# Optimization experiments

Hardware: AMD Instinct MI355X
Metric: run time of the kernel (lower is better)

The kernel has to match this reference:

```python
import jax, jax.numpy as jnp
import numpy as np

H = 512      # hidden_size
NH = 8       # num_attention_heads
HD = H // NH # attention_head_size
B, S = 2, 4096


def setup_inputs() -> dict:
    key = jax.random.key(0)
    ks = jax.random.split(key, 9)
    sc = 1.0 / np.sqrt(H)
    return {
        "hidden_states": jax.random.normal(ks[0], (B, S, H), dtype=jnp.float32),
        "Wq": jax.random.normal(ks[1], (H, H), dtype=jnp.float32) * sc,
        "bq": jnp.zeros((H,), dtype=jnp.float32),
        "Wk": jax.random.normal(ks[2], (H, H), dtype=jnp.float32) * sc,
        "bk": jnp.zeros((H,), dtype=jnp.float32),
        "Wv": jax.random.normal(ks[3], (H, H), dtype=jnp.float32) * sc,
        "bv": jnp.zeros((H,), dtype=jnp.float32),
        "Wo": jax.random.normal(ks[4], (H, H), dtype=jnp.float32) * sc,
        "bo": jnp.zeros((H,), dtype=jnp.float32),
    }


def reference(hidden_states, Wq, bq, Wk, bk, Wv, bv, Wo, bo):
    # QKV projections (nn.Linear: x @ W.T + b)
    def split_heads(x):  # [B,S,H] -> [B,NH,S,HD]
        return x.reshape(B, S, NH, HD).transpose(0, 2, 1, 3)

    q = split_heads(hidden_states @ Wq.T + bq)
    k = split_heads(hidden_states @ Wk.T + bk)
    v = split_heads(hidden_states @ Wv.T + bv)

    scores = jnp.einsum("bhqd,bhkd->bhqk", q, k) / np.sqrt(HD)
    probs = jax.nn.softmax(scores, axis=-1)  # dropout is identity in eval
    ctx = jnp.einsum("bhqk,bhkd->bhqd", probs, v)
    ctx = ctx.transpose(0, 2, 1, 3).reshape(B, S, H)
    return ctx @ Wo.T + bo
```

## Files before the change

kernel.cpp:

```cpp
#include <hip/hip_runtime.h>
#include <hip/hip_bf16.h>
#include <math.h>


typedef __bf16 bf16;
typedef __bf16 bf16x2v __attribute__((ext_vector_type(2)));
typedef __bf16 bf16x4 __attribute__((ext_vector_type(4)));
typedef __bf16 bf16x8 __attribute__((ext_vector_type(8)));
typedef float  f32x4  __attribute__((ext_vector_type(4)));
typedef unsigned int u32x2 __attribute__((ext_vector_type(2)));
typedef unsigned int u32x4 __attribute__((ext_vector_type(4)));

#define MFMA16(a, b, c) __builtin_amdgcn_mfma_f32_16x16x32_bf16((a), (b), (c), 0, 0, 0)

__device__ __forceinline__ void gll16(const bf16* g, bf16* l) {
    __builtin_amdgcn_global_load_lds(
        (const __attribute__((address_space(1))) void*)g,
        (__attribute__((address_space(3))) void*)l, 16, 0, 0);
}

__device__ __forceinline__ unsigned int cvtpk(float lo, float hi) {
    unsigned int r;
    asm("v_cvt_pk_bf16_f32 %0, %1, %2" : "=v"(r) : "v"(lo), "v"(hi));
    return r;
}

__global__ __launch_bounds__(256) void cvt_f32_bf16(const float* __restrict__ src,
                                                    bf16* __restrict__ dst, int n) {
    int i = (blockIdx.x * 256 + threadIdx.x) * 4;
    if (i >= n) return;
    float4 v = *reinterpret_cast<const float4*>(src + i);
    bf16x4 o = {(bf16)v.x, (bf16)v.y, (bf16)v.z, (bf16)v.w};
    *reinterpret_cast<bf16x4*>(dst + i) = o;
}

__global__ __launch_bounds__(256) void cvt_w4(const float* __restrict__ a,
                                              const float* __restrict__ b,
                                              const float* __restrict__ c,
                                              const float* __restrict__ d,
                                              bf16* __restrict__ out) {
    const int y = blockIdx.y;
    const float* src = (y == 0) ? a : (y == 1) ? b : (y == 2) ? c : d;
    int i = (blockIdx.x * 256 + threadIdx.x) * 4;
    float4 v = *reinterpret_cast<const float4*>(src + i);
    bf16x4 o = {(bf16)v.x, (bf16)v.y, (bf16)v.z, (bf16)v.w};
    *reinterpret_cast<bf16x4*>(out + y * 262144 + i) = o;
}

template <int MODE>
__global__ __launch_bounds__(256) void gemm_bt(const bf16* __restrict__ A,
                                               const bf16* __restrict__ W,
                                               const float* __restrict__ b0,
                                               const float* __restrict__ b1,
                                               const float* __restrict__ b2,
                                               bf16* __restrict__ dstbf,
                                               float* __restrict__ dstf) {
    __shared__ bf16 sA[128 * 64];
    __shared__ bf16 sB[128 * 64];

    const int tid = threadIdx.x;
    const int w   = tid >> 6;
    const int l   = tid & 63;

    int bx, by, bz;
    if (MODE == 0) {
        int lin = (blockIdx.x & 7) * 96 + (blockIdx.x >> 3);
        const int rem = lin % 12;
        bx = rem & 3; bz = rem >> 2; by = lin / 12;
    } else {
        int lin = (blockIdx.x & 7) * 32 + (blockIdx.x >> 3);
        bx = lin & 3; by = lin >> 2; bz = 0;
    }
    const int m0 = by * 128;
    const int n0 = bx * 128;
    const int z  = bz;

    const bf16*  Wz   = (MODE == 0) ? (W + z * 262144) : W;
    const float* bias = (MODE == 0) ? (z == 0 ? b0 : (z == 1 ? b1 : b2)) : b0;
    const float  scale = (MODE == 0 && z == 0) ? 0.125f * 1.4426950408889634f : 1.0f;

    const int wr = (w >> 1) * 64, wc = (w & 1) * 64;
    const int fr = l & 15, fg = l >> 4;

    const int srow0 = tid >> 3;
    const int sgr   = (tid & 7) ^ (srow0 & 7);
    const int ldso  = srow0 * 64 + (tid & 7) * 8;

    f32x4 acc[4][4];
    const f32x4 zero = {0.f, 0.f, 0.f, 0.f};
#pragma unroll
    for (int i = 0; i < 4; i++)
#pragma unroll
        for (int j = 0; j < 4; j++) acc[i][j] = zero;

    for (int kt = 0; kt < 512; kt += 64) {
        __syncthreads();
#pragma unroll
        for (int p = 0; p < 4; p++) {
            const int row = srow0 + 32 * p;
            gll16(A  + (m0 + row) * 512 + kt + sgr * 8, &sA[p * 2048 + ldso]);
            gll16(Wz + (n0 + row) * 512 + kt + sgr * 8, &sB[p * 2048 + ldso]);
        }
        __syncthreads();

#pragma unroll
        for (int ks = 0; ks < 2; ks++) {
            bf16x8 af[4], bfg[4];
#pragma unroll
            for (int mi = 0; mi < 4; mi++)
                af[mi] = *reinterpret_cast<const bf16x8*>(
                    &sA[(wr + mi * 16 + fr) * 64 + (((4 * ks + fg) ^ (fr & 7)) << 3)]);
#pragma unroll
            for (int ni = 0; ni < 4; ni++)
                bfg[ni] = *reinterpret_cast<const bf16x8*>(
                    &sB[(wc + ni * 16 + fr) * 64 + (((4 * ks + fg) ^ (fr & 7)) << 3)]);
#pragma unroll
            for (int mi = 0; mi < 4; mi++)
#pragma unroll
                for (int ni = 0; ni < 4; ni++)
                    acc[mi][ni] = MFMA16(af[mi], bfg[ni], acc[mi][ni]);
        }
    }

#pragma unroll
    for (int mi = 0; mi < 4; mi++) {
#pragma unroll
        for (int ni = 0; ni < 4; ni++) {
            const int gcol = n0 + wc + ni * 16 + fr;
            const float bc = bias[gcol];
#pragma unroll
            for (int r = 0; r < 4; r++) {
                const int grow = m0 + wr + mi * 16 + fg * 4 + r;
                float v = acc[mi][ni][r] + bc;
                if (MODE == 0) {
                    v *= scale;
                    const int bb = grow >> 12, s = grow & 4095;
                    const int hh = gcol >> 6, dd = gcol & 63;
                    size_t idx;
                    if (z == 2) {
                        idx = (size_t)2 * 4194304 +
                              ((size_t)((bb * 8 + hh) * 64 + dd)) * 4096 + s;
                    } else {
                        idx = (size_t)z * 4194304 +
                              ((size_t)((bb * 8 + hh) * 4096 + s) << 6) + dd;
                    }
                    dstbf[idx] = (bf16)v;
                } else {
                    dstf[grow * 512 + gcol] = v;
                }
            }
        }
    }
}

__global__ __launch_bounds__(256, 2) void attn_kernel(const bf16* __restrict__ Q,
                                                      const bf16* __restrict__ K,
                                                      const bf16* __restrict__ Vt,
                                                      bf16* __restrict__ ctx) {
    __shared__ bf16 sKb[2][4096];
    __shared__ bf16 sVb[2][4096];

    const int tid = threadIdx.x;
    const int w   = tid >> 6;
    const int l   = tid & 63;
    const int fr  = l & 15, fg = l >> 4;

    int n = blockIdx.y * 32 + blockIdx.x;
    n = (n & 7) * 64 + (n >> 3);
    const int bh  = n >> 5;
    const int q0  = (n & 31) * 128;
    const size_t base = (size_t)bh * 262144;

    const int srow0 = tid >> 3;
    const int sgr   = (tid & 7) ^ (srow0 & 7);
    const int ldso  = srow0 * 64 + (tid & 7) * 8;

    const int ko0 = fr * 64 + (((0 + fg) ^ (fr & 7)) << 3);
    const int ko1 = fr * 64 + (((4 + fg) ^ (fr & 7)) << 3);

#define STAGE(buf, tt)                                                              \
    do {                                                                            \
        _Pragma("unroll")                                                           \
        for (int p = 0; p < 2; p++) {                                               \
            const int row_ = srow0 + 32 * p;                                        \
            gll16(K  + base + (size_t)((tt) + row_) * 64 + sgr * 8,                 \
                  &sKb[buf][p * 2048 + ldso]);                                      \
            gll16(Vt + base + (size_t)row_ * 4096 + (tt) + sgr * 8,                 \
                  &sVb[buf][p * 2048 + ldso]);                                      \
        }                                                                           \
    } while (0)

#define QK_TILE(kb_)                                                                \
    do {                                                                            \
        _Pragma("unroll")                                                           \
        for (int kvb = 0; kvb < 4; kvb++) {                                         \
            const bf16x8 kf0 = *reinterpret_cast<const bf16x8*>((kb_) + ko0 + kvb * 1024); \
            const bf16x8 kf1 = *reinterpret_cast<const bf16x8*>((kb_) + ko1 + kvb * 1024); \
            _Pragma("unroll")                                                       \
            for (int qb = 0; qb < 2; qb++) {                                        \
                sc[kvb][qb] = MFMA16(kf0, qf[0][qb], zero);                         \
                sc[kvb][qb] = MFMA16(kf1, qf[1][qb], sc[kvb][qb]);                  \
            }                                                                       \
        }                                                                           \
    } while (0)

#define PV_TILE()                                                                   \
    do {                                                                            \
        _Pragma("unroll")                                                           \
        for (int ks = 0; ks < 2; ks++) {                                            \
            _Pragma("unroll")                                                       \
            for (int qb = 0; qb < 2; qb++)                                          \
                lacc[qb] = MFMA16(ones, pf[ks][qb], lacc[qb]);                      \
            _Pragma("unroll")                                                       \
            for (int db = 0; db < 4; db++)                                          \
                _Pragma("unroll")                                                   \
                for (int qb = 0; qb < 2; qb++)                                      \
                    o[db][qb] = MFMA16(vf[ks][db], pf[ks][qb], o[db][qb]);          \
        }                                                                           \
    } while (0)

#define VF_READ(vb_)                                                                \
    do {                                                                            \
        _Pragma("unroll")                                                           \
        for (int db = 0; db < 4; db++) {                                            \
            vf[0][db] = *reinterpret_cast<const bf16x8*>((vb_) + ko0 + db * 1024);  \
            vf[1][db] = *reinterpret_cast<const bf16x8*>((vb_) + ko1 + db * 1024);  \
        }                                                                           \
    } while (0)

#define SOFTMAX_PACK()                                                              \
    do {                                                                            \
        _Pragma("unroll")                                                           \
        for (int qb = 0; qb < 2; qb++) {                                            \
            unsigned int c[4][2];                                                   \
            _Pragma("unroll")                                                       \
            for (int kvb = 0; kvb < 4; kvb++) {                                     \
                const float p0 = __builtin_amdgcn_exp2f(sc[kvb][qb][0]);            \
                const float p1 = __builtin_amdgcn_exp2f(sc[kvb][qb][1]);            \
                const float p2 = __builtin_amdgcn_exp2f(sc[kvb][qb][2]);            \
                const float p3 = __builtin_amdgcn_exp2f(sc[kvb][qb][3]);            \
                c[kvb][0] = cvtpk(p0, p1);                                          \
                c[kvb][1] = cvtpk(p2, p3);                                          \
            }                                                                       \
            _Pragma("unroll")                                                       \
            for (int ks = 0; ks < 2; ks++) {                                        \
                unsigned int a0 = c[2 * ks][0], b0 = c[2 * ks + 1][0];              \
                unsigned int a1 = c[2 * ks][1], b1 = c[2 * ks + 1][1];              \
                asm("v_permlane32_swap_b32 %0, %1" : "+v"(a0), "+v"(b0));           \
                asm("v_permlane16_swap_b32 %0, %1" : "+v"(a0), "+v"(b0));           \
                asm("v_permlane32_swap_b32 %0, %1" : "+v"(a1), "+v"(b1));           \
                asm("v_permlane16_swap_b32 %0, %1" : "+v"(a1), "+v"(b1));           \
                u32x4 uu = {a0, a1, b0, b1};                                        \
                pf[ks][qb] = __builtin_bit_cast(bf16x8, uu);                        \
            }                                                                       \
        }                                                                           \
    } while (0)

#define BODY(KBUF, tt)                                                              \
    do {                                                                            \
        __syncthreads();                                                            \
        STAGE((KBUF) ^ 1, (tt) + 64);                                               \
        __builtin_amdgcn_s_setprio(1);                                              \
        QK_TILE(sKb[KBUF]);                                                         \
        PV_TILE();                                                                  \
        __builtin_amdgcn_s_setprio(0);                                              \
        VF_READ(sVb[KBUF]);                                                         \
        SOFTMAX_PACK();                                                             \
    } while (0)

    bf16x8 qf[2][2];
#pragma unroll
    for (int qb = 0; qb < 2; qb++)
#pragma unroll
        for (int ks = 0; ks < 2; ks++)
            qf[ks][qb] = *reinterpret_cast<const bf16x8*>(
                Q + base + (size_t)(q0 + 32 * w + 16 * qb + fr) * 64 + ks * 32 + fg * 8);

    const bf16 one = (bf16)1.0f;
    const bf16x8 ones = {one, one, one, one, one, one, one, one};

    const f32x4 zero = {0.f, 0.f, 0.f, 0.f};
    f32x4 o[4][2];
#pragma unroll
    for (int db = 0; db < 4; db++)
#pragma unroll
        for (int qb = 0; qb < 2; qb++) o[db][qb] = zero;
    f32x4 lacc[2] = {zero, zero};

    f32x4  sc[4][2];
    bf16x8 vf[2][4];
    bf16x8 pf[2][2];

    STAGE(0, 0);
    __syncthreads();
    STAGE(1, 64);
    QK_TILE(sKb[0]);
    VF_READ(sVb[0]);
    SOFTMAX_PACK();

    int t = 64;
    for (int i = 0; i < 31; i++, t += 128) {
        BODY(1, t);
        BODY(0, t + 64);
    }

    __syncthreads();
    __builtin_amdgcn_s_setprio(1);
    QK_TILE(sKb[1]);
    PV_TILE();
    __builtin_amdgcn_s_setprio(0);
    VF_READ(sVb[1]);
    SOFTMAX_PACK();
    __builtin_amdgcn_s_setprio(1);
    PV_TILE();
    __builtin_amdgcn_s_setprio(0);

    const int bb = bh >> 3, hh = bh & 7;
#pragma unroll
    for (int qb = 0; qb < 2; qb++) {
        const float inv = 1.0f / lacc[qb][0];
        const int s = q0 + 32 * w + 16 * qb + fr;
#pragma unroll
        for (int db = 0; db < 4; db++) {
            u32x2 pr = {cvtpk(o[db][qb][0] * inv, o[db][qb][1] * inv),
                        cvtpk(o[db][qb][2] * inv, o[db][qb][3] * inv)};
            *reinterpret_cast<u32x2*>(
                &ctx[((size_t)(bb * 4096 + s)) * 512 + hh * 64 + db * 16 + 4 * fg]) = pr;
        }
    }
#undef STAGE
#undef QK_TILE
#undef PV_TILE
#undef VF_READ
#undef SOFTMAX_PACK
#undef BODY
}

extern "C" void kernel_launch(void* const* d_in, const int* in_sizes, int n_in,
                              void* d_out, int out_size, void* d_ws, size_t ws_size,
                              hipStream_t stream) {
    const float* X  = (const float*)d_in[0];
    const float* Wq = (const float*)d_in[1];
    const float* bq = (const float*)d_in[2];
    const float* Wk = (const float*)d_in[3];
    const float* bk = (const float*)d_in[4];
    const float* Wv = (const float*)d_in[5];
    const float* bv = (const float*)d_in[6];
    const float* Wo = (const float*)d_in[7];
    const float* bo = (const float*)d_in[8];
    float* out = (float*)d_out;

    bf16* ws  = (bf16*)d_ws;
    bf16* Xbf = ws;
    bf16* Wqb = Xbf + 4194304;
    bf16* Qb  = Wqb + 4 * 262144;
    bf16* Kb  = Qb + 4194304;
    bf16* Vtb = Kb + 4194304;
    bf16* Ctx = Vtb + 4194304;

    cvt_f32_bf16<<<4096, 256, 0, stream>>>(X, Xbf, 4194304);
    cvt_w4<<<dim3(256, 4), 256, 0, stream>>>(Wq, Wk, Wv, Wo, Wqb);

    gemm_bt<0><<<768, 256, 0, stream>>>(Xbf, Wqb, bq, bk, bv, Qb, nullptr);

    attn_kernel<<<dim3(32, 16), 256, 0, stream>>>(Qb, Kb, Vtb, Ctx);

    gemm_bt<1><<<256, 256, 0, stream>>>(Ctx, Wqb + 3 * 262144, bo,
                                        nullptr, nullptr, nullptr, out);
}
```

Baseline: 139.0 us.

## Software-pipeline softmax exp with next tile's QK MFMAs using double-buffered scores

```diff
diff --git a/kernel.cpp b/kernel.cpp
--- a/kernel.cpp
+++ b/kernel.cpp
@@ -190,7 +190,7 @@
         }                                                                           \
     } while (0)
 
-#define QK_TILE(kb_)                                                                \
+#define QKSM_TILE(kb_, SCN, SCO)                                                    \
     do {                                                                            \
         _Pragma("unroll")                                                           \
         for (int kvb = 0; kvb < 4; kvb++) {                                         \
@@ -198,54 +198,27 @@
             const bf16x8 kf1 = *reinterpret_cast<const bf16x8*>((kb_) + ko1 + kvb * 1024); \
             _Pragma("unroll")                                                       \
             for (int qb = 0; qb < 2; qb++) {                                        \
-                sc[kvb][qb] = MFMA16(kf0, qf[0][qb], zero);                         \
-                sc[kvb][qb] = MFMA16(kf1, qf[1][qb], sc[kvb][qb]);                  \
+                SCN[kvb][qb] = MFMA16(kf0, qf[0][qb], zero);                        \
+                SCN[kvb][qb] = MFMA16(kf1, qf[1][qb], SCN[kvb][qb]);                \
             }                                                                       \
-        }                                                                           \
-    } while (0)
-
-#define PV_TILE()                                                                   \
-    do {                                                                            \
-        _Pragma("unroll")                                                           \
-        for (int ks = 0; ks < 2; ks++) {                                            \
-            _Pragma("unroll")                                                       \
-            for (int qb = 0; qb < 2; qb++)                                          \
-                lacc[qb] = MFMA16(ones, pf[ks][qb], lacc[qb]);                      \
-            _Pragma("unroll")                                                       \
-            for (int db = 0; db < 4; db++)                                          \
-                _Pragma("unroll")                                                   \
-                for (int qb = 0; qb < 2; qb++)                                      \
-                    o[db][qb] = MFMA16(vf[ks][db], pf[ks][qb], o[db][qb]);          \
-        }                                                                           \
-    } while (0)
-
-#define VF_READ(vb_)                                                                \
-    do {                                                                            \
-        _Pragma("unroll")                                                           \
-        for (int db = 0; db < 4; db++) {                                            \
-            vf[0][db] = *reinterpret_cast<const bf16x8*>((vb_) + ko0 + db * 1024);  \
-            vf[1][db] = *reinterpret_cast<const bf16x8*>((vb_) + ko1 + db * 1024);  \
-        }                                                                           \
-    } while (0)
-
-#define SOFTMAX_PACK()                                                              \
+            _Pragma("unroll")                                                       \
+            for (int qb = 0; qb < 2; qb++) {                                        \
+                cc[qb][kvb][0] = cvtpk(__builtin_amdgcn_exp2f(SCO[kvb][qb][0]),     \
+                                       __builtin_amdgcn_exp2f(SCO[kvb][qb][1]));    \
+                cc[qb][kvb][1] = cvtpk(__builtin_amdgcn_exp2f(SCO[kvb][qb][2]),     \
+                                       __builtin_amdgcn_exp2f(SCO[kvb][qb][3]));    \
+            }                                                                       \
+        }                                                                           \
+    } while (0)
+
+#define PERMPACK()                                                                  \
     do {                                                                            \
         _Pragma("unroll")                                                           \
         for (int qb = 0; qb < 2; qb++) {                                            \
-            unsigned int c[4][2];                                                   \
-            _Pragma("unroll")                                                       \
-            for (int kvb = 0; kvb < 4; kvb++) {                                     \
-                const float p0 = __builtin_amdgcn_exp2f(sc[kvb][qb][0]);            \
-                const float p1 = __builtin_amdgcn_exp2f(sc[kvb][qb][1]);            \
-                const float p2 = __builtin_amdgcn_exp2f(sc[kvb][qb][2]);            \
-                const float p3 = __builtin_amdgcn_exp2f(sc[kvb][qb][3]);            \
-                c[kvb][0] = cvtpk(p0, p1);                                          \
-                c[kvb][1] = cvtpk(p2, p3);                                          \
-            }                                                                       \
             _Pragma("unroll")                                                       \
             for (int ks = 0; ks < 2; ks++) {                                        \
-                unsigned int a0 = c[2 * ks][0], b0 = c[2 * ks + 1][0];              \
-                unsigned int a1 = c[2 * ks][1], b1 = c[2 * ks + 1][1];              \
+                unsigned int a0 = cc[qb][2 * ks][0], b0 = cc[qb][2 * ks + 1][0];    \
+                unsigned int a1 = cc[qb][2 * ks][1], b1 = cc[qb][2 * ks + 1][1];    \
                 asm("v_permlane32_swap_b32 %0, %1" : "+v"(a0), "+v"(b0));           \
                 asm("v_permlane16_swap_b32 %0, %1" : "+v"(a0), "+v"(b0));           \
                 asm("v_permlane32_swap_b32 %0, %1" : "+v"(a1), "+v"(b1));           \
@@ -256,16 +229,54 @@
         }                                                                           \
     } while (0)
 
-#define BODY(KBUF, tt)                                                              \
+#define PV_TILE()                                                                   \
+    do {                                                                            \
+        _Pragma("unroll")                                                           \
+        for (int ks = 0; ks < 2; ks++) {                                            \
+            _Pragma("unroll")                                                       \
+            for (int qb = 0; qb < 2; qb++)                                          \
+                lacc[qb] = MFMA16(ones, pf[ks][qb], lacc[qb]);                      \
+            _Pragma("unroll")                                                       \
+            for (int db = 0; db < 4; db++)                                          \
+                _Pragma("unroll")                                                   \
+                for (int qb = 0; qb < 2; qb++)                                      \
+                    o[db][qb] = MFMA16(vf[ks][db], pf[ks][qb], o[db][qb]);          \
+        }                                                                           \
+    } while (0)
+
+#define VF_READ(vb_)                                                                \
+    do {                                                                            \
+        _Pragma("unroll")                                                           \
+        for (int db = 0; db < 4; db++) {                                            \
+            vf[0][db] = *reinterpret_cast<const bf16x8*>((vb_) + ko0 + db * 1024);  \
+            vf[1][db] = *reinterpret_cast<const bf16x8*>((vb_) + ko1 + db * 1024);  \
+        }                                                                           \
+    } while (0)
+
+#define SOFTMAX_FULL(SC)                                                            \
+    do {                                                                            \
+        _Pragma("unroll")                                                           \
+        for (int qb = 0; qb < 2; qb++)                                              \
+            _Pragma("unroll")                                                       \
+            for (int kvb = 0; kvb < 4; kvb++) {                                     \
+                cc[qb][kvb][0] = cvtpk(__builtin_amdgcn_exp2f(SC[kvb][qb][0]),      \
+                                       __builtin_amdgcn_exp2f(SC[kvb][qb][1]));     \
+                cc[qb][kvb][1] = cvtpk(__builtin_amdgcn_exp2f(SC[kvb][qb][2]),      \
+                                       __builtin_amdgcn_exp2f(SC[kvb][qb][3]));     \
+            }                                                                       \
+        PERMPACK();                                                                 \
+    } while (0)
+
+#define BODY(KBUF, tt, SCN, SCO)                                                    \
     do {                                                                            \
         __syncthreads();                                                            \
         STAGE((KBUF) ^ 1, (tt) + 64);                                               \
         __builtin_amdgcn_s_setprio(1);                                              \
-        QK_TILE(sKb[KBUF]);                                                         \
+        QKSM_TILE(sKb[KBUF], SCN, SCO);                                             \
+        PERMPACK();                                                                 \
         PV_TILE();                                                                  \
         __builtin_amdgcn_s_setprio(0);                                              \
         VF_READ(sVb[KBUF]);                                                         \
-        SOFTMAX_PACK();                                                             \
     } while (0)
 
     bf16x8 qf[2][2];
@@ -287,30 +298,42 @@
         for (int qb = 0; qb < 2; qb++) o[db][qb] = zero;
     f32x4 lacc[2] = {zero, zero};
 
-    f32x4  sc[4][2];
+    f32x4  scA[4][2], scB[4][2];
     bf16x8 vf[2][4];
     bf16x8 pf[2][2];
+    unsigned int cc[2][4][2];
 
     STAGE(0, 0);
     __syncthreads();
     STAGE(1, 64);
-    QK_TILE(sKb[0]);
+    {
+#pragma unroll
+        for (int kvb = 0; kvb < 4; kvb++) {
+            const bf16x8 kf0 = *reinterpret_cast<const bf16x8*>(sKb[0] + ko0 + kvb * 1024);
+            const bf16x8 kf1 = *reinterpret_cast<const bf16x8*>(sKb[0] + ko1 + kvb * 1024);
+#pragma unroll
+            for (int qb = 0; qb < 2; qb++) {
+                scA[kvb][qb] = MFMA16(kf0, qf[0][qb], zero);
+                scA[kvb][qb] = MFMA16(kf1, qf[1][qb], scA[kvb][qb]);
+            }
+        }
+    }
     VF_READ(sVb[0]);
-    SOFTMAX_PACK();
 
     int t = 64;
     for (int i = 0; i < 31; i++, t += 128) {
-        BODY(1, t);
-        BODY(0, t + 64);
+        BODY(1, t, scB, scA);
+        BODY(0, t + 64, scA, scB);
     }
 
     __syncthreads();
     __builtin_amdgcn_s_setprio(1);
-    QK_TILE(sKb[1]);
+    QKSM_TILE(sKb[1], scB, scA);
+    PERMPACK();
     PV_TILE();
     __builtin_amdgcn_s_setprio(0);
     VF_READ(sVb[1]);
-    SOFTMAX_PACK();
+    SOFTMAX_FULL(scB);
     __builtin_amdgcn_s_setprio(1);
     PV_TILE();
     __builtin_amdgcn_s_setprio(0);
@@ -329,10 +352,11 @@
         }
     }
 #undef STAGE
-#undef QK_TILE
+#undef QKSM_TILE
+#undef PERMPACK
 #undef PV_TILE
 #undef VF_READ
-#undef SOFTMAX_PACK
+#undef SOFTMAX_FULL
 #undef BODY
 }
 
```

Result: no change. 136.3 us (-1.9%).
